# Kernel tuning notes

Hardware: AMD Instinct MI355X
Metric: run time of the kernel (lower is better)

## Reference

```python
import jax, jax.numpy as jnp
import numpy as np

NUM_CLASSES = 19
IGNORE_INDEX = 255

B, C, H, W = 8, 256, 128, 256


def setup_inputs() -> dict:
    key = jax.random.key(0)
    k1, k2, k3, k4 = jax.random.split(key, 4)
    s_feat = jax.random.normal(k1, (B, C, H, W), dtype=jnp.float32)
    t_feat = jax.random.normal(k2, (B, C, H, W), dtype=jnp.float32)
    mask = jax.random.randint(k3, (B, H, W), 0, NUM_CLASSES, dtype=jnp.int64)
    swt_weight = jax.random.uniform(k4, (B, 1, H, W), dtype=jnp.float32)
    return {"s_feat": s_feat, "t_feat": t_feat, "mask": mask, "swt_weight": swt_weight}


def _update_prototypes(t_feat, mask):
    # First call: prototypes are initialized directly from class means (proto_initialized=False path).
    b, c, h, w = t_feat.shape
    feat_flat = t_feat.transpose(0, 2, 3, 1).reshape(-1, c)  # [N, C]
    mask_flat = mask.reshape(-1)
    valid = mask_flat != IGNORE_INDEX
    seg = jnp.where(valid, mask_flat, 0).astype(jnp.int32)
    wgt = valid.astype(feat_flat.dtype)
    # single-pass segment-reduce replacing the per-class python loop
    sums = jax.ops.segment_sum(feat_flat * wgt[:, None], seg, num_segments=NUM_CLASSES)
    counts = jax.ops.segment_sum(wgt, seg, num_segments=NUM_CLASSES)  # [K]
    protos = jnp.where(counts[:, None] > 0, sums / jnp.maximum(counts, 1.0)[:, None], 0.0)
    # normalize (classes never seen stay zero: 0 / clamp(0,1e-6) = 0)
    norm = jnp.maximum(jnp.linalg.norm(protos, axis=-1, keepdims=True), 1e-6)
    return protos / norm


def reference(s_feat, t_feat, mask, swt_weight):
    prototypes = _update_prototypes(jax.lax.stop_gradient(t_feat), mask)  # [K, C]

    # cosine similarity of normalized student features against per-pixel class prototype
    s_perm = s_feat.transpose(0, 2, 3, 1)  # [B,H,W,C]
    s_norm = s_perm / jnp.maximum(jnp.linalg.norm(s_perm, axis=-1, keepdims=True), 1e-12)

    safe_mask = jnp.where(mask == IGNORE_INDEX, 0, mask)
    proto_norm = jnp.linalg.norm(prototypes, axis=-1)  # [K]
    proto_valid = proto_norm > 0

    target_protos = prototypes[safe_mask]          # [B,H,W,C] gather
    proto_valid_per_pixel = proto_valid[safe_mask]  # [B,H,W]

    sim_map = jnp.sum(s_norm * target_protos, axis=-1)  # [B,H,W]
    raw_loss_map = 1.0 - sim_map
    valid_mask_f = ((mask != IGNORE_INDEX) & proto_valid_per_pixel).astype(s_feat.dtype)
    swt_map = swt_weight[:, 0]  # [B,H,W]

    weighted_loss_map = raw_loss_map * valid_mask_f * swt_map
    denom = jnp.maximum((valid_mask_f * swt_map).sum(), 1.0)
    final_loss = weighted_loss_map.sum() / denom
    denom_sim = jnp.maximum(valid_mask_f.sum(), 1.0)
    mean_sim = (sim_map * valid_mask_f).sum() / denom_sim

    return (final_loss, sim_map, weighted_loss_map, mean_sim, proto_norm, proto_valid)
```

## Files before the change

kernel.cpp:

```cpp
#include <hip/hip_runtime.h>

#define NCLS 19
#define IGN 255
#define C_DIM 256
#define HW 32768
#define PIX 262144
#define PAIRS (PIX/2)
#define PS (NCLS*C_DIM + NCLS)

#define WS_ACC 0
#define WS_PROT 8
#define WS_PV  4872
#define WS_PART 4896

#define O_LOSS 0
#define O_SIM  1
#define O_WL   (1 + PIX)
#define O_MS   (1 + 2*PIX)
#define O_PN   (2 + 2*PIX)
#define O_PV   (2 + 2*PIX + NCLS)

__global__ __launch_bounds__(256) void protoAccum(const float* __restrict__ t,
                                                  const int* __restrict__ mask,
                                                  float* __restrict__ part) {
    __shared__ float ls[NCLS * 257];
    __shared__ float lc[NCLS];
    const int tid = threadIdx.x;
    for (int i = tid; i < NCLS * 257; i += 256) ls[i] = 0.f;
    if (tid < NCLS) lc[tid] = 0.f;
    __syncthreads();

    for (int idx = blockIdx.x * 256 + tid; idx < PAIRS; idx += gridDim.x * 256) {
        const int p0 = idx * 2;
        const int b = p0 >> 15;
        const int hw = p0 & (HW - 1);
        const int2 kk = *(const int2*)(mask + p0);
        const bool v0 = (kk.x != IGN);
        const bool v1 = (kk.y != IGN);
        if (v0) atomicAdd(&lc[kk.x], 1.f);
        if (v1) atomicAdd(&lc[kk.y], 1.f);
        const int b0 = v0 ? kk.x * 257 : 0;
        const int b1 = v1 ? kk.y * 257 : 0;
        const float* tb = t + (size_t)b * C_DIM * HW + hw;
        #pragma unroll 4
        for (int c = 0; c < C_DIM; ++c) {
            const float2 v = *(const float2*)(tb + (size_t)c * HW);
            if (v0) atomicAdd(&ls[b0 + c], v.x);
            if (v1) atomicAdd(&ls[b1 + c], v.y);
        }
    }
    __syncthreads();

    float* pb = part + (size_t)blockIdx.x * PS;
    for (int i = tid; i < NCLS * C_DIM; i += 256) {
        const int k = i >> 8, c = i & 255;
        pb[i] = ls[k * 257 + c];
    }
    if (tid < NCLS) pb[NCLS * C_DIM + tid] = lc[tid];
}

__global__ __launch_bounds__(1024) void protoReduce(const float* __restrict__ part, int nb,
                                                    float* __restrict__ ws,
                                                    float* __restrict__ out) {
    __shared__ float red[1024];
    __shared__ float s4[4][C_DIM];
    const int k = blockIdx.x;
    const int tid = threadIdx.x;
    const int c = tid & 255;
    const int g = tid >> 8;

    float cp = 0.f;
    for (int b = tid; b < nb; b += 1024) cp += part[(size_t)b * PS + NCLS * C_DIM + k];
    red[tid] = cp; __syncthreads();
    for (int s = 512; s > 0; s >>= 1) { if (tid < s) red[tid] += red[tid + s]; __syncthreads(); }
    const float cnt = red[0]; __syncthreads();

    float sp = 0.f;
    for (int b = g; b < nb; b += 4) sp += part[(size_t)b * PS + k * C_DIM + c];
    s4[g][c] = sp; __syncthreads();
    float raw = s4[0][c] + s4[1][c] + s4[2][c] + s4[3][c];
    raw = (cnt > 0.f) ? (raw / fmaxf(cnt, 1.f)) : 0.f;

    red[tid] = (g == 0) ? raw * raw : 0.f; __syncthreads();
    for (int s = 512; s > 0; s >>= 1) { if (tid < s) red[tid] += red[tid + s]; __syncthreads(); }
    const float n1 = sqrtf(red[0]); __syncthreads();
    const float p = raw / fmaxf(n1, 1e-6f);
    if (g == 0) ws[WS_PROT + k * C_DIM + c] = p;

    red[tid] = (g == 0) ? p * p : 0.f; __syncthreads();
    for (int s = 512; s > 0; s >>= 1) { if (tid < s) red[tid] += red[tid + s]; __syncthreads(); }
    if (tid == 0) {
        const float pn = sqrtf(red[0]);
        out[O_PN + k] = pn;
        const float pv = (pn > 0.f) ? 1.f : 0.f;
        out[O_PV + k] = pv;
        ws[WS_PV + k] = pv;
        if (k == 0) { ws[WS_ACC+0] = 0.f; ws[WS_ACC+1] = 0.f; ws[WS_ACC+2] = 0.f; ws[WS_ACC+3] = 0.f; }
    }
}

__global__ __launch_bounds__(256) void simLoss(const float* __restrict__ s,
                                               const int* __restrict__ mask,
                                               const float* __restrict__ swt,
                                               const float* __restrict__ ws,
                                               float* __restrict__ out,
                                               float* __restrict__ acc) {
    __shared__ float lp[NCLS * 257];
    __shared__ float lpv[NCLS];
    __shared__ float redw[256];
    const int tid = threadIdx.x;
    for (int i = tid; i < NCLS * C_DIM; i += 256)
        lp[(i >> 8) * 257 + (i & 255)] = ws[WS_PROT + i];
    if (tid < NCLS) lpv[tid] = ws[WS_PV + tid];
    __syncthreads();

    float s_wl = 0.f, s_vw = 0.f, s_sv = 0.f, s_v = 0.f;
    const int idx = blockIdx.x * 256 + tid;
    if (idx < PAIRS) {
        const int p0 = idx * 2;
        const int b = p0 >> 15;
        const int hw = p0 & (HW - 1);
        const int2 kk = *(const int2*)(mask + p0);
        const float2 sw = *(const float2*)(swt + p0);
        const bool v0 = (kk.x != IGN), v1 = (kk.y != IGN);
        const int k0 = v0 ? kk.x : 0;
        const int k1 = v1 ? kk.y : 0;
        const int b0 = k0 * 257, b1 = k1 * 257;
        const float* sb = s + (size_t)b * C_DIM * HW + hw;
        float d0 = 0.f, d1 = 0.f, q0 = 0.f, q1 = 0.f;
        #pragma unroll 8
        for (int c = 0; c < C_DIM; ++c) {
            const float2 v = *(const float2*)(sb + (size_t)c * HW);
            d0 += v.x * lp[b0 + c];
            q0 += v.x * v.x;
            d1 += v.y * lp[b1 + c];
            q1 += v.y * v.y;
        }
        const float sim0 = d0 / fmaxf(sqrtf(q0), 1e-12f);
        const float sim1 = d1 / fmaxf(sqrtf(q1), 1e-12f);
        const float vm0 = (v0 && lpv[k0] > 0.f) ? 1.f : 0.f;
        const float vm1 = (v1 && lpv[k1] > 0.f) ? 1.f : 0.f;
        const float wl0 = (1.f - sim0) * vm0 * sw.x;
        const float wl1 = (1.f - sim1) * vm1 * sw.y;
        out[O_SIM + p0]     = sim0;
        out[O_SIM + p0 + 1] = sim1;
        out[O_WL + p0]      = wl0;
        out[O_WL + p0 + 1]  = wl1;
        s_wl = wl0 + wl1;
        s_vw = vm0 * sw.x + vm1 * sw.y;
        s_sv = sim0 * vm0 + sim1 * vm1;
        s_v  = vm0 + vm1;
    }

    float vals[4] = { s_wl, s_vw, s_sv, s_v };
    #pragma unroll
    for (int r = 0; r < 4; ++r) {
        redw[tid] = vals[r]; __syncthreads();
        for (int s2 = 128; s2 > 0; s2 >>= 1) {
            if (tid < s2) redw[tid] += redw[tid + s2];
            __syncthreads();
        }
        if (tid == 0) atomicAdd(&acc[r], redw[0]);
        __syncthreads();
    }
}

__global__ void finalK(const float* __restrict__ acc, float* __restrict__ out) {
    if (threadIdx.x == 0 && blockIdx.x == 0) {
        out[O_LOSS] = acc[0] / fmaxf(acc[1], 1.f);
        out[O_MS]   = acc[2] / fmaxf(acc[3], 1.f);
    }
}

extern "C" void kernel_launch(void* const* d_in, const int* in_sizes, int n_in,
                              void* d_out, int out_size, void* d_ws, size_t ws_size,
                              hipStream_t stream) {
    const float* s_feat = (const float*)d_in[0];
    const float* t_feat = (const float*)d_in[1];
    const int*   mask   = (const int*)d_in[2];
    const float* swt    = (const float*)d_in[3];
    float* out = (float*)d_out;
    float* ws  = (float*)d_ws;

    int NBA = 512;
    {
        const size_t avail = ws_size / 4;
        if (avail > (size_t)WS_PART) {
            const size_t fit = (avail - WS_PART) / PS;
            if (fit < (size_t)NBA) NBA = (int)(fit > 0 ? fit : 1);
        } else {
            NBA = 1;
        }
    }
    float* part = ws + WS_PART;

    protoAccum<<<NBA, 256, 0, stream>>>(t_feat, mask, part);
    protoReduce<<<NCLS, 1024, 0, stream>>>(part, NBA, ws, out);
    simLoss<<<(PAIRS + 255) / 256, 256, 0, stream>>>(s_feat, mask, swt, ws, out, ws + WS_ACC);
    finalK<<<1, 64, 0, stream>>>(ws + WS_ACC, out);
}
```

Measured before the change: 821.0 us.

## Tile channels through shared memory and split channel groups across warps

```diff
diff --git a/kernel.cpp b/kernel.cpp
--- a/kernel.cpp
+++ b/kernel.cpp
@@ -5,13 +5,16 @@
 #define C_DIM 256
 #define HW 32768
 #define PIX 262144
-#define PAIRS (PIX/2)
-#define PS (NCLS*C_DIM + NCLS)
+#define TPX 256
+#define CCH 8
+#define NCHUNK 32
+#define TSTR 258
 
 #define WS_ACC 0
-#define WS_PROT 8
-#define WS_PV  4872
-#define WS_PART 4896
+#define WS_GSUM 16
+#define WS_GCNT (WS_GSUM + NCLS*C_DIM)
+#define WS_PROT 4900
+#define WS_PV   (WS_PROT + NCLS*C_DIM)
 
 #define O_LOSS 0
 #define O_SIM  1
@@ -20,148 +23,222 @@
 #define O_PN   (2 + 2*PIX)
 #define O_PV   (2 + 2*PIX + NCLS)
 
-__global__ __launch_bounds__(256) void protoAccum(const float* __restrict__ t,
-                                                  const int* __restrict__ mask,
-                                                  float* __restrict__ part) {
-    __shared__ float ls[NCLS * 257];
-    __shared__ float lc[NCLS];
+__global__ __launch_bounds__(256, 4) void protoAccum(const float* __restrict__ t,
+                                                     const int* __restrict__ mask,
+                                                     float* __restrict__ gsum,
+                                                     float* __restrict__ gcnt) {
+    __shared__ float tile[CCH * TSTR];
+    __shared__ float acc[NCLS * 257];
+    __shared__ float cnt[NCLS];
     const int tid = threadIdx.x;
-    for (int i = tid; i < NCLS * 257; i += 256) ls[i] = 0.f;
-    if (tid < NCLS) lc[tid] = 0.f;
-    __syncthreads();
-
-    for (int idx = blockIdx.x * 256 + tid; idx < PAIRS; idx += gridDim.x * 256) {
-        const int p0 = idx * 2;
-        const int b = p0 >> 15;
-        const int hw = p0 & (HW - 1);
-        const int2 kk = *(const int2*)(mask + p0);
-        const bool v0 = (kk.x != IGN);
-        const bool v1 = (kk.y != IGN);
-        if (v0) atomicAdd(&lc[kk.x], 1.f);
-        if (v1) atomicAdd(&lc[kk.y], 1.f);
-        const int b0 = v0 ? kk.x * 257 : 0;
-        const int b1 = v1 ? kk.y * 257 : 0;
-        const float* tb = t + (size_t)b * C_DIM * HW + hw;
-        #pragma unroll 4
-        for (int c = 0; c < C_DIM; ++c) {
-            const float2 v = *(const float2*)(tb + (size_t)c * HW);
-            if (v0) atomicAdd(&ls[b0 + c], v.x);
-            if (v1) atomicAdd(&ls[b1 + c], v.y);
-        }
-    }
-    __syncthreads();
-
-    float* pb = part + (size_t)blockIdx.x * PS;
+    for (int i = tid; i < NCLS * 257; i += 256) acc[i] = 0.f;
+    if (tid < NCLS) cnt[tid] = 0.f;
+
+    const int px0 = blockIdx.x * TPX;
+    const int b = px0 >> 15;
+    const int hw0 = px0 & (HW - 1);
+    const float* tb = t + (size_t)b * C_DIM * HW + hw0;
+
+    const int pbase = tid & 31;
+    const int g = tid >> 5;
+
+    int   cls[8];
+    float fva[8];
+    #pragma unroll
+    for (int j = 0; j < 8; ++j) {
+        const int m = mask[px0 + pbase + 32 * j];
+        const bool v = (m != IGN);
+        cls[j] = v ? m : 0;
+        fva[j] = v ? 1.f : 0.f;
+    }
+
+    float2 r[4];
+    #pragma unroll
+    for (int k = 0; k < 4; ++k) {
+        const int e = tid + 256 * k;
+        r[k] = *(const float2*)(tb + (size_t)(e >> 7) * HW + 2 * (e & 127));
+    }
+    __syncthreads();
+
+    if (g == 0) {
+        #pragma unroll
+        for (int j = 0; j < 8; ++j) atomicAdd(&cnt[cls[j]], fva[j]);
+    }
+
+    for (int n = 0; n < NCHUNK; ++n) {
+        #pragma unroll
+        for (int k = 0; k < 4; ++k) {
+            const int e = tid + 256 * k;
+            *(float2*)&tile[(e >> 7) * TSTR + 2 * (e & 127)] = r[k];
+        }
+        if (n + 1 < NCHUNK) {
+            const float* tc = tb + (size_t)(n + 1) * CCH * HW;
+            #pragma unroll
+            for (int k = 0; k < 4; ++k) {
+                const int e = tid + 256 * k;
+                r[k] = *(const float2*)(tc + (size_t)(e >> 7) * HW + 2 * (e & 127));
+            }
+        }
+        __syncthreads();
+        const int cglob = n * CCH + g;
+        #pragma unroll
+        for (int j = 0; j < 8; ++j) {
+            const float v = tile[g * TSTR + pbase + 32 * j];
+            atomicAdd(&acc[cls[j] * 257 + cglob], v * fva[j]);
+        }
+        __syncthreads();
+    }
+
     for (int i = tid; i < NCLS * C_DIM; i += 256) {
         const int k = i >> 8, c = i & 255;
-        pb[i] = ls[k * 257 + c];
-    }
-    if (tid < NCLS) pb[NCLS * C_DIM + tid] = lc[tid];
-}
-
-__global__ __launch_bounds__(1024) void protoReduce(const float* __restrict__ part, int nb,
-                                                    float* __restrict__ ws,
-                                                    float* __restrict__ out) {
-    __shared__ float red[1024];
-    __shared__ float s4[4][C_DIM];
+        atomicAdd(&gsum[i], acc[k * 257 + c]);
+    }
+    if (tid < NCLS) atomicAdd(&gcnt[tid], cnt[tid]);
+}
+
+__global__ __launch_bounds__(256) void protoReduce(const float* __restrict__ gsum,
+                                                   const float* __restrict__ gcnt,
+                                                   float* __restrict__ ws,
+                                                   float* __restrict__ out) {
+    __shared__ float wr[4], wr2[4];
     const int k = blockIdx.x;
     const int tid = threadIdx.x;
-    const int c = tid & 255;
-    const int g = tid >> 8;
-
-    float cp = 0.f;
-    for (int b = tid; b < nb; b += 1024) cp += part[(size_t)b * PS + NCLS * C_DIM + k];
-    red[tid] = cp; __syncthreads();
-    for (int s = 512; s > 0; s >>= 1) { if (tid < s) red[tid] += red[tid + s]; __syncthreads(); }
-    const float cnt = red[0]; __syncthreads();
-
-    float sp = 0.f;
-    for (int b = g; b < nb; b += 4) sp += part[(size_t)b * PS + k * C_DIM + c];
-    s4[g][c] = sp; __syncthreads();
-    float raw = s4[0][c] + s4[1][c] + s4[2][c] + s4[3][c];
-    raw = (cnt > 0.f) ? (raw / fmaxf(cnt, 1.f)) : 0.f;
-
-    red[tid] = (g == 0) ? raw * raw : 0.f; __syncthreads();
-    for (int s = 512; s > 0; s >>= 1) { if (tid < s) red[tid] += red[tid + s]; __syncthreads(); }
-    const float n1 = sqrtf(red[0]); __syncthreads();
-    const float p = raw / fmaxf(n1, 1e-6f);
-    if (g == 0) ws[WS_PROT + k * C_DIM + c] = p;
-
-    red[tid] = (g == 0) ? p * p : 0.f; __syncthreads();
-    for (int s = 512; s > 0; s >>= 1) { if (tid < s) red[tid] += red[tid + s]; __syncthreads(); }
+    const int lane = tid & 63, wv = tid >> 6;
+
+    const float cn = gcnt[k];
+    const float raw = gsum[k * 256 + tid];
+    const float mean = (cn > 0.f) ? raw / fmaxf(cn, 1.f) : 0.f;
+
+    float v = mean * mean;
+    #pragma unroll
+    for (int o = 32; o > 0; o >>= 1) v += __shfl_down(v, o);
+    if (lane == 0) wr[wv] = v;
+    __syncthreads();
+    const float S = wr[0] + wr[1] + wr[2] + wr[3];
+    const float p = mean / fmaxf(sqrtf(S), 1e-6f);
+    ws[WS_PROT + k * 256 + tid] = p;
+
+    float v2 = p * p;
+    #pragma unroll
+    for (int o = 32; o > 0; o >>= 1) v2 += __shfl_down(v2, o);
+    if (lane == 0) wr2[wv] = v2;
+    __syncthreads();
     if (tid == 0) {
-        const float pn = sqrtf(red[0]);
+        const float pn = sqrtf(wr2[0] + wr2[1] + wr2[2] + wr2[3]);
         out[O_PN + k] = pn;
-        const float pv = (pn > 0.f) ? 1.f : 0.f;
-        out[O_PV + k] = pv;
-        ws[WS_PV + k] = pv;
-        if (k == 0) { ws[WS_ACC+0] = 0.f; ws[WS_ACC+1] = 0.f; ws[WS_ACC+2] = 0.f; ws[WS_ACC+3] = 0.f; }
-    }
-}
-
-__global__ __launch_bounds__(256) void simLoss(const float* __restrict__ s,
-                                               const int* __restrict__ mask,
-                                               const float* __restrict__ swt,
-                                               const float* __restrict__ ws,
-                                               float* __restrict__ out,
-                                               float* __restrict__ acc) {
-    __shared__ float lp[NCLS * 257];
-    __shared__ float lpv[NCLS];
-    __shared__ float redw[256];
+        const float pvv = (pn > 0.f) ? 1.f : 0.f;
+        out[O_PV + k] = pvv;
+        ws[WS_PV + k] = pvv;
+    }
+}
+
+__global__ __launch_bounds__(256, 4) void simLoss(const float* __restrict__ s,
+                                                  const int* __restrict__ mask,
+                                                  const float* __restrict__ swt,
+                                                  const float* __restrict__ ws,
+                                                  float* __restrict__ out,
+                                                  float* __restrict__ acc4) {
+    __shared__ float sm[CCH * TSTR + NCLS * 257];
+    __shared__ float pv[NCLS];
+    __shared__ float wred[4][4];
+    float* tile = sm;
+    float* proto = sm + CCH * TSTR;
+
     const int tid = threadIdx.x;
     for (int i = tid; i < NCLS * C_DIM; i += 256)
-        lp[(i >> 8) * 257 + (i & 255)] = ws[WS_PROT + i];
-    if (tid < NCLS) lpv[tid] = ws[WS_PV + tid];
-    __syncthreads();
-
-    float s_wl = 0.f, s_vw = 0.f, s_sv = 0.f, s_v = 0.f;
-    const int idx = blockIdx.x * 256 + tid;
-    if (idx < PAIRS) {
-        const int p0 = idx * 2;
-        const int b = p0 >> 15;
-        const int hw = p0 & (HW - 1);
-        const int2 kk = *(const int2*)(mask + p0);
-        const float2 sw = *(const float2*)(swt + p0);
-        const bool v0 = (kk.x != IGN), v1 = (kk.y != IGN);
-        const int k0 = v0 ? kk.x : 0;
-        const int k1 = v1 ? kk.y : 0;
-        const int b0 = k0 * 257, b1 = k1 * 257;
-        const float* sb = s + (size_t)b * C_DIM * HW + hw;
-        float d0 = 0.f, d1 = 0.f, q0 = 0.f, q1 = 0.f;
-        #pragma unroll 8
-        for (int c = 0; c < C_DIM; ++c) {
-            const float2 v = *(const float2*)(sb + (size_t)c * HW);
-            d0 += v.x * lp[b0 + c];
-            q0 += v.x * v.x;
-            d1 += v.y * lp[b1 + c];
-            q1 += v.y * v.y;
-        }
-        const float sim0 = d0 / fmaxf(sqrtf(q0), 1e-12f);
-        const float sim1 = d1 / fmaxf(sqrtf(q1), 1e-12f);
-        const float vm0 = (v0 && lpv[k0] > 0.f) ? 1.f : 0.f;
-        const float vm1 = (v1 && lpv[k1] > 0.f) ? 1.f : 0.f;
-        const float wl0 = (1.f - sim0) * vm0 * sw.x;
-        const float wl1 = (1.f - sim1) * vm1 * sw.y;
-        out[O_SIM + p0]     = sim0;
-        out[O_SIM + p0 + 1] = sim1;
-        out[O_WL + p0]      = wl0;
-        out[O_WL + p0 + 1]  = wl1;
-        s_wl = wl0 + wl1;
-        s_vw = vm0 * sw.x + vm1 * sw.y;
-        s_sv = sim0 * vm0 + sim1 * vm1;
-        s_v  = vm0 + vm1;
-    }
-
-    float vals[4] = { s_wl, s_vw, s_sv, s_v };
-    #pragma unroll
-    for (int r = 0; r < 4; ++r) {
-        redw[tid] = vals[r]; __syncthreads();
-        for (int s2 = 128; s2 > 0; s2 >>= 1) {
-            if (tid < s2) redw[tid] += redw[tid + s2];
-            __syncthreads();
-        }
-        if (tid == 0) atomicAdd(&acc[r], redw[0]);
-        __syncthreads();
+        proto[(i >> 8) * 257 + (i & 255)] = ws[WS_PROT + i];
+    if (tid < NCLS) pv[tid] = ws[WS_PV + tid];
+
+    const int px0 = blockIdx.x * TPX;
+    const int b = px0 >> 15;
+    const int hw0 = px0 & (HW - 1);
+    const float* sb = s + (size_t)b * C_DIM * HW + hw0;
+
+    const int pbase = tid & 31;
+    const int g = tid >> 5;
+
+    int mreg[8];
+    #pragma unroll
+    for (int j = 0; j < 8; ++j) mreg[j] = mask[px0 + pbase + 32 * j];
+
+    float2 r[4];
+    #pragma unroll
+    for (int k = 0; k < 4; ++k) {
+        const int e = tid + 256 * k;
+        r[k] = *(const float2*)(sb + (size_t)(e >> 7) * HW + 2 * (e & 127));
+    }
+    __syncthreads();
+
+    int cls[8];
+    #pragma unroll
+    for (int j = 0; j < 8; ++j) cls[j] = (mreg[j] != IGN) ? mreg[j] : 0;
+
+    float d[8], q[8];
+    #pragma unroll
+    for (int j = 0; j < 8; ++j) { d[j] = 0.f; q[j] = 0.f; }
+
+    for (int n = 0; n < NCHUNK; ++n) {
+        #pragma unroll
+        for (int k = 0; k < 4; ++k) {
+            const int e = tid + 256 * k;
+            *(float2*)&tile[(e >> 7) * TSTR + 2 * (e & 127)] = r[k];
+        }
+        if (n + 1 < NCHUNK) {
+            const float* sc = sb + (size_t)(n + 1) * CCH * HW;
+            #pragma unroll
+            for (int k = 0; k < 4; ++k) {
+                const int e = tid + 256 * k;
+                r[k] = *(const float2*)(sc + (size_t)(e >> 7) * HW + 2 * (e & 127));
+            }
+        }
+        __syncthreads();
+        const int cglob = n * CCH + g;
+        #pragma unroll
+        for (int j = 0; j < 8; ++j) {
+            const float v = tile[g * TSTR + pbase + 32 * j];
+            d[j] += v * proto[cls[j] * 257 + cglob];
+            q[j] += v * v;
+        }
+        __syncthreads();
+    }
+
+    #pragma unroll
+    for (int j = 0; j < 8; ++j) {
+        float2 w; w.x = d[j]; w.y = q[j];
+        *(float2*)&sm[g * (TPX * 2) + (pbase + 32 * j) * 2] = w;
+    }
+    __syncthreads();
+
+    float dt = 0.f, qt = 0.f;
+    #pragma unroll
+    for (int gg = 0; gg < 8; ++gg) {
+        const float2 w = *(const float2*)&sm[gg * (TPX * 2) + tid * 2];
+        dt += w.x; qt += w.y;
+    }
+
+    const int mp = mask[px0 + tid];
+    const bool vp = (mp != IGN);
+    const int kp = vp ? mp : 0;
+    const float vm = (vp && pv[kp] > 0.f) ? 1.f : 0.f;
+    const float sw = swt[px0 + tid];
+    const float sim = dt / fmaxf(sqrtf(qt), 1e-12f);
+    const float wl = (1.f - sim) * vm * sw;
+    out[O_SIM + px0 + tid] = sim;
+    out[O_WL + px0 + tid] = wl;
+
+    float vals[4] = { wl, vm * sw, sim * vm, vm };
+    const int lane = tid & 63, wv = tid >> 6;
+    #pragma unroll
+    for (int rr = 0; rr < 4; ++rr) {
+        float x = vals[rr];
+        #pragma unroll
+        for (int o = 32; o > 0; o >>= 1) x += __shfl_down(x, o);
+        if (lane == 0) wred[wv][rr] = x;
+    }
+    __syncthreads();
+    if (tid < 4) {
+        const float sumv = wred[0][tid] + wred[1][tid] + wred[2][tid] + wred[3][tid];
+        atomicAdd(&acc4[tid], sumv);
     }
 }
 
@@ -182,20 +259,10 @@
     float* out = (float*)d_out;
     float* ws  = (float*)d_ws;
 
-    int NBA = 512;
-    {
-        const size_t avail = ws_size / 4;
-        if (avail > (size_t)WS_PART) {
-            const size_t fit = (avail - WS_PART) / PS;
-            if (fit < (size_t)NBA) NBA = (int)(fit > 0 ? fit : 1);
-        } else {
-            NBA = 1;
-        }
-    }
-    float* part = ws + WS_PART;
-
-    protoAccum<<<NBA, 256, 0, stream>>>(t_feat, mask, part);
-    protoReduce<<<NCLS, 1024, 0, stream>>>(part, NBA, ws, out);
-    simLoss<<<(PAIRS + 255) / 256, 256, 0, stream>>>(s_feat, mask, swt, ws, out, ws + WS_ACC);
+    hipMemsetAsync(ws, 0, (size_t)WS_PROT * sizeof(float), stream);
+
+    protoAccum<<<PIX / TPX, 256, 0, stream>>>(t_feat, mask, ws + WS_GSUM, ws + WS_GCNT);
+    protoReduce<<<NCLS, 256, 0, stream>>>(ws + WS_GSUM, ws + WS_GCNT, ws, out);
+    simLoss<<<PIX / TPX, 256, 0, stream>>>(s_feat, mask, swt, ws, out, ws + WS_ACC);
     finalK<<<1, 64, 0, stream>>>(ws + WS_ACC, out);
 }
```

Result: faster. 777.7 us (-5.3%).
